# Optimization experiments

Measured on AMD Instinct MI355X. Metric: run time of the kernel, lower is better.

Reference implementation:

```python
import jax, jax.numpy as jnp
import numpy as np

N_NODES = 50000
N_EDGES = 800000
NUM_GRAPHS = 250
NODES_PER_GRAPH = 200  # max_len for to_dense_batch
IN_DIM = 128
H1 = 128
H2 = 128
LSTM_H = 128
OUT_DIM = 2
NEG_SLOPE = 0.2  # PyG GATConv default leaky relu slope


def setup_inputs() -> dict:
    key = jax.random.key(0)
    ks = jax.random.split(key, 16)
    x = jax.random.normal(ks[0], (N_NODES, IN_DIM), dtype=jnp.float32)
    edge_index = jax.random.randint(ks[1], (2, N_EDGES), 0, N_NODES, dtype=jnp.int32)
    batch = (jnp.arange(N_NODES, dtype=jnp.int32) // NODES_PER_GRAPH)
    g = lambda k, shp, fan: jax.random.normal(k, shp, dtype=jnp.float32) / np.sqrt(fan)
    return {
        "x": x,
        "edge_index": edge_index,
        "batch": batch,
        "W_gat": g(ks[2], (IN_DIM, H1), IN_DIM),
        "a_src": g(ks[3], (H1,), H1),
        "a_dst": g(ks[4], (H1,), H1),
        "b_gat": jnp.zeros((H1,), jnp.float32),
        "W_gcn": g(ks[5], (H1, H2), H1),
        "b_gcn": jnp.zeros((H2,), jnp.float32),
        "W_ih": g(ks[6], (4 * LSTM_H, H2), H2),
        "W_hh": g(ks[7], (4 * LSTM_H, LSTM_H), LSTM_H),
        "b_ih": jnp.zeros((4 * LSTM_H,), jnp.float32),
        "b_hh": jnp.zeros((4 * LSTM_H,), jnp.float32),
        "W_fc": g(ks[8], (LSTM_H, OUT_DIM), LSTM_H),
        "b_fc": jnp.zeros((OUT_DIM,), jnp.float32),
    }


def _add_self_loops(edge_index, n):
    loop = jnp.arange(n, dtype=edge_index.dtype)
    src = jnp.concatenate([edge_index[0], loop])
    dst = jnp.concatenate([edge_index[1], loop])
    return src, dst


def _gat_conv(x, edge_index, W, a_src, a_dst, b):
    n = x.shape[0]
    h = x @ W                                  # [N, H1]
    src, dst = _add_self_loops(edge_index, n)
    alpha_s = h @ a_src                        # [N]
    alpha_d = h @ a_dst
    e = alpha_s[src] + alpha_d[dst]            # [E+N]
    e = jnp.where(e > 0, e, NEG_SLOPE * e)     # leaky relu
    # softmax over edges sharing the same destination node
    m = jax.ops.segment_max(e, dst, num_segments=n)
    ex = jnp.exp(e - m[dst])
    denom = jax.ops.segment_sum(ex, dst, num_segments=n)
    alpha = ex / denom[dst]
    out = jax.ops.segment_sum(h[src] * alpha[:, None], dst, num_segments=n)
    return out + b


def _gcn_conv(x, edge_index, W, b):
    n = x.shape[0]
    h = x @ W                                  # [N, H2]
    src, dst = _add_self_loops(edge_index, n)
    deg = jax.ops.segment_sum(jnp.ones_like(dst, dtype=h.dtype), dst, num_segments=n)
    dinv = jax.lax.rsqrt(jnp.maximum(deg, 1.0))
    coef = dinv[src] * dinv[dst]               # symmetric normalization
    out = jax.ops.segment_sum(h[src] * coef[:, None], dst, num_segments=n)
    return out + b


def _to_dense_batch(x, batch, num_graphs, max_len):
    n = x.shape[0]
    ones = jnp.ones((n,), jnp.int32)
    counts = jax.ops.segment_sum(ones, batch, num_segments=num_graphs)
    starts = jnp.cumsum(counts) - counts
    pos = jnp.arange(n, dtype=jnp.int32) - starts[batch]
    padded = jnp.zeros((num_graphs, max_len, x.shape[1]), x.dtype)
    padded = padded.at[batch, pos].set(x)
    return padded, counts


def _lstm_last_hidden(padded, lengths, W_ih, W_hh, b_ih, b_hh):
    B, T, D = padded.shape
    H = W_hh.shape[1]
    xs = jnp.swapaxes(padded, 0, 1)            # [T, B, D]

    def step(carry, x_t):
        h, c = carry
        gates = x_t @ W_ih.T + b_ih + h @ W_hh.T + b_hh
        i, f, g, o = jnp.split(gates, 4, axis=-1)
        c = jax.nn.sigmoid(f) * c + jax.nn.sigmoid(i) * jnp.tanh(g)
        h = jax.nn.sigmoid(o) * jnp.tanh(c)
        return (h, c), h

    init = (jnp.zeros((B, H), padded.dtype), jnp.zeros((B, H), padded.dtype))
    _, hs = jax.lax.scan(step, init, xs)       # hs: [T, B, H]
    # packed-sequence semantics: hidden state at each graph's last valid step
    return hs[lengths - 1, jnp.arange(B)]


def reference(x, edge_index, batch, W_gat, a_src, a_dst, b_gat, W_gcn, b_gcn,
              W_ih, W_hh, b_ih, b_hh, W_fc, b_fc):
    h = jax.nn.relu(_gat_conv(x, edge_index, W_gat, a_src, a_dst, b_gat))
    h = jax.nn.relu(_gcn_conv(h, edge_index, W_gcn, b_gcn))
    padded, lengths = _to_dense_batch(h, batch, NUM_GRAPHS, NODES_PER_GRAPH)
    g_rep = _lstm_last_hidden(padded, lengths, W_ih, W_hh, b_ih, b_hh)
    return g_rep @ W_fc + b_fc
```

## Files before the change

kernel.cpp:

```cpp
#include <hip/hip_runtime.h>
#include <cstddef>

#define NN 50000
#define NE 800000
#define NG 250
#define TT 200
#define DD 128
#define GH 512
#define NEG_SLOPE 0.2f
#define NCHUNK 4
#define CLEN 50
#define CAP 128
#define PSTRIDE 136

typedef __attribute__((ext_vector_type(8))) short bf16x8;
typedef __attribute__((ext_vector_type(4))) float f32x4;

static __device__ __forceinline__ float fsig(float x) { return 1.0f / (1.0f + __expf(-x)); }
static __device__ __forceinline__ float ftanh(float x) {
    float e = __expf(2.0f * x);
    return 1.0f - 2.0f / (e + 1.0f);
}
static __device__ __forceinline__ unsigned short f2bf(float f) {
    unsigned int u = __float_as_uint(f);
    return (unsigned short)((u + 0x7fffu + ((u >> 16) & 1u)) >> 16);
}
static __device__ __forceinline__ float bf2f(unsigned short b) {
    return __uint_as_float(((unsigned int)b) << 16);
}

static __device__ __forceinline__ void gll16(const float* src, float* ldsdst) {
    __builtin_amdgcn_global_load_lds(
        (const __attribute__((address_space(1))) void*)src,
        (__attribute__((address_space(3))) void*)ldsdst, 16, 0, 0);
}

__global__ void k_init(int* cnt, int* gstart, int n, int ng1) {
    int i = blockIdx.x * 256 + threadIdx.x;
    if (i < n) cnt[i] = 1;
    if (i < ng1) gstart[i] = n;
}

__global__ void k_transpose2(const float* __restrict__ inA, float* __restrict__ outA,
                             const float* __restrict__ inB, float* __restrict__ outB) {
    int b = blockIdx.x, k = threadIdx.x;
    if (b < DD) outA[b * DD + k] = inA[k * DD + b];
    else { int n = b - DD; outB[n * DD + k] = inB[k * DD + n]; }
}

__global__ __launch_bounds__(256) void k_gemm(
    const float* __restrict__ A, const float* __restrict__ B, float* __restrict__ C,
    int M, int N, int t0, int clen, int rowsPerGraph,
    const float* __restrict__ bias1, const float* __restrict__ bias2,
    unsigned short* __restrict__ Cbf,
    float* __restrict__ as_out, float* __restrict__ ad_out,
    const float* __restrict__ a_src, const float* __restrict__ a_dst)
{
    __shared__ float4 As[2][1024];
    __shared__ float4 Bs[2][1024];
    const int tid = threadIdx.x;
    const int wv = tid >> 6;
    const int m0 = blockIdx.x * 128, n0 = blockIdx.y * 128;
    const int tr = tid >> 4, tc = tid & 15;

    float acc[8][8];
    #pragma unroll
    for (int i = 0; i < 8; ++i)
        #pragma unroll
        for (int j = 0; j < 8; ++j) acc[i][j] = 0.f;

    auto stageA = [&](int buf, int k0) {
        #pragma unroll
        for (int it = 0; it < 4; ++it) {
            int f4 = it * 256 + tid;
            int r = f4 >> 3;
            int c4s = (f4 & 7) ^ (r & 7);
            int gr = m0 + r;
            float* dst = (float*)&As[buf][it * 256 + wv * 64];
            if (gr < M) {
                int flat = (gr / clen) * rowsPerGraph + t0 + (gr % clen);
                gll16(A + (size_t)flat * DD + k0 + c4s * 4, dst);
            }
        }
    };
    auto stageB = [&](int buf, int k0) {
        #pragma unroll
        for (int it = 0; it < 4; ++it) {
            int f4 = it * 256 + tid;
            int r = f4 >> 3;
            int c4s = (f4 & 7) ^ (r & 7);
            int gn = n0 + r;
            float* dst = (float*)&Bs[buf][it * 256 + wv * 64];
            if (gn < N) gll16(B + (size_t)gn * DD + k0 + c4s * 4, dst);
        }
    };

    stageA(0, 0); stageB(0, 0);
    __syncthreads();
    int buf = 0;
    const int axor = tr & 7;
    const int bxor = tc & 7;
    for (int ks = 0; ks < 4; ++ks) {
        if (ks < 3) { stageA(buf ^ 1, (ks + 1) * 32); stageB(buf ^ 1, (ks + 1) * 32); }
        const float4* Af = &As[buf][0];
        const float4* Bf = &Bs[buf][0];
        #pragma unroll 1
        for (int k4 = 0; k4 < 8; ++k4) {
            float4 a[8], b[8];
            #pragma unroll
            for (int i = 0; i < 8; ++i) a[i] = Af[(tr + i * 16) * 8 + (k4 ^ axor)];
            #pragma unroll
            for (int j = 0; j < 8; ++j) b[j] = Bf[(tc + j * 16) * 8 + (k4 ^ bxor)];
            #pragma unroll
            for (int i = 0; i < 8; ++i)
                #pragma unroll
                for (int j = 0; j < 8; ++j)
                    acc[i][j] += a[i].x * b[j].x + a[i].y * b[j].y + a[i].z * b[j].z + a[i].w * b[j].w;
        }
        __syncthreads();
        buf ^= 1;
    }

    if (as_out) {
        float asv[8], adv[8];
        #pragma unroll
        for (int j = 0; j < 8; ++j) { asv[j] = a_src[tc + 16 * j]; adv[j] = a_dst[tc + 16 * j]; }
        #pragma unroll
        for (int i = 0; i < 8; ++i) {
            float s = 0.f, d = 0.f;
            #pragma unroll
            for (int j = 0; j < 8; ++j) { s += acc[i][j] * asv[j]; d += acc[i][j] * adv[j]; }
            #pragma unroll
            for (int off = 1; off < 16; off <<= 1) { s += __shfl_xor(s, off); d += __shfl_xor(d, off); }
            int gr = m0 + tr + i * 16;
            if (tc == 0 && gr < M) { as_out[gr] = s; ad_out[gr] = d; }
        }
    }

    #pragma unroll
    for (int i = 0; i < 8; ++i) {
        int gr = m0 + tr + i * 16;
        if (gr >= M) continue;
        #pragma unroll
        for (int j = 0; j < 8; ++j) {
            int gn = n0 + tc + j * 16;
            if (gn >= N) continue;
            float v = acc[i][j];
            if (bias1) v += bias1[gn];
            if (bias2) v += bias2[gn];
            if (Cbf) Cbf[(size_t)gr * N + gn] = f2bf(v);
            else     C[(size_t)gr * N + gn] = v;
        }
    }
}

__global__ __launch_bounds__(256) void k_gemm_mx(
    const float* __restrict__ A, const float* __restrict__ Bw, float* __restrict__ C,
    int M, int N, const float* __restrict__ bias1, const float* __restrict__ bias2)
{
    __shared__ float4 As[4096];
    const int tid = threadIdx.x;
    const int wv = tid >> 6;
    const int l = tid & 63;
    const int m0 = blockIdx.x * 128, n0 = blockIdx.y * 128;
    const int wr = (wv >> 1) * 64, wc = (wv & 1) * 64;
    const int lr = l & 15, kg = l >> 4;

    #pragma unroll
    for (int it = 0; it < 16; ++it) {
        int f4 = it * 256 + tid;
        int r = f4 >> 5, c4 = f4 & 31;
        int c4s = c4 ^ (r & 7);
        int gr = m0 + r;
        float* dst = (float*)&As[it * 256 + wv * 64];
        if (gr < M) gll16(A + (size_t)gr * DD + c4s * 4, dst);
    }

    bf16x8 bh[4][4];
    #pragma unroll
    for (int ct = 0; ct < 4; ++ct) {
        const float* brow = Bw + (size_t)(n0 + wc + ct * 16 + lr) * DD;
        #pragma unroll
        for (int ks = 0; ks < 4; ++ks) {
            float4 f0 = *(const float4*)(brow + ks * 32 + kg * 8);
            float4 f1 = *(const float4*)(brow + ks * 32 + kg * 8 + 4);
            float ff[8] = {f0.x, f0.y, f0.z, f0.w, f1.x, f1.y, f1.z, f1.w};
            #pragma unroll
            for (int j = 0; j < 8; ++j) bh[ct][ks][j] = (short)f2bf(ff[j]);
        }
    }
    __syncthreads();

    f32x4 acc[4][4];
    #pragma unroll
    for (int rt = 0; rt < 4; ++rt)
        #pragma unroll
        for (int ct = 0; ct < 4; ++ct) acc[rt][ct] = (f32x4){0.f, 0.f, 0.f, 0.f};

    #pragma unroll 1
    for (int ks = 0; ks < 4; ++ks) {
        bf16x8 ahi[4], alo[4];
        #pragma unroll
        for (int rt = 0; rt < 4; ++rt) {
            int row = wr + rt * 16 + lr;
            int qb = ks * 8 + kg * 2;
            float4 f0 = As[row * 32 + (qb ^ (row & 7))];
            float4 f1 = As[row * 32 + ((qb + 1) ^ (row & 7))];
            float ff[8] = {f0.x, f0.y, f0.z, f0.w, f1.x, f1.y, f1.z, f1.w};
            #pragma unroll
            for (int j = 0; j < 8; ++j) {
                unsigned short hi = f2bf(ff[j]);
                ahi[rt][j] = (short)hi;
                alo[rt][j] = (short)f2bf(ff[j] - bf2f(hi));
            }
        }
        #pragma unroll
        for (int rt = 0; rt < 4; ++rt)
            #pragma unroll
            for (int ct = 0; ct < 4; ++ct) {
                acc[rt][ct] = __builtin_amdgcn_mfma_f32_16x16x32_bf16(ahi[rt], bh[ct][ks], acc[rt][ct], 0, 0, 0);
                acc[rt][ct] = __builtin_amdgcn_mfma_f32_16x16x32_bf16(alo[rt], bh[ct][ks], acc[rt][ct], 0, 0, 0);
            }
    }

    #pragma unroll
    for (int ct = 0; ct < 4; ++ct) {
        const float* brow = Bw + (size_t)(n0 + wc + ct * 16 + lr) * DD;
        #pragma unroll
        for (int ks = 0; ks < 4; ++ks) {
            float4 f0 = *(const float4*)(brow + ks * 32 + kg * 8);
            float4 f1 = *(const float4*)(brow + ks * 32 + kg * 8 + 4);
            float ff[8] = {f0.x, f0.y, f0.z, f0.w, f1.x, f1.y, f1.z, f1.w};
            #pragma unroll
            for (int j = 0; j < 8; ++j)
                bh[ct][ks][j] = (short)f2bf(ff[j] - bf2f(f2bf(ff[j])));
        }
    }

    #pragma unroll 1
    for (int ks = 0; ks < 4; ++ks) {
        bf16x8 ahi[4];
        #pragma unroll
        for (int rt = 0; rt < 4; ++rt) {
            int row = wr + rt * 16 + lr;
            int qb = ks * 8 + kg * 2;
            float4 f0 = As[row * 32 + (qb ^ (row & 7))];
            float4 f1 = As[row * 32 + ((qb + 1) ^ (row & 7))];
            float ff[8] = {f0.x, f0.y, f0.z, f0.w, f1.x, f1.y, f1.z, f1.w};
            #pragma unroll
            for (int j = 0; j < 8; ++j) ahi[rt][j] = (short)f2bf(ff[j]);
        }
        #pragma unroll
        for (int rt = 0; rt < 4; ++rt)
            #pragma unroll
            for (int ct = 0; ct < 4; ++ct)
                acc[rt][ct] = __builtin_amdgcn_mfma_f32_16x16x32_bf16(ahi[rt], bh[ct][ks], acc[rt][ct], 0, 0, 0);
    }

    #pragma unroll
    for (int ct = 0; ct < 4; ++ct) {
        int col = n0 + wc + ct * 16 + lr;
        float bsum = bias1[col] + bias2[col];
        #pragma unroll
        for (int rt = 0; rt < 4; ++rt) {
            #pragma unroll
            for (int r = 0; r < 4; ++r) {
                int row = m0 + wr + rt * 16 + kg * 4 + r;
                if (row < M) C[(size_t)row * N + col] = acc[rt][ct][r] + bsum;
            }
        }
    }
}

__global__ void k_hist(const int* __restrict__ ei, int* cnt, int E) {
    int e = blockIdx.x * 256 + threadIdx.x;
    if (e < E) atomicAdd(&cnt[ei[E + e]], 1);
}

__global__ __launch_bounds__(256) void k_scan1(const int* __restrict__ cnt, int* __restrict__ fill,
                                               int* __restrict__ bsum, int n) {
    __shared__ int wsum[4];
    int tid = threadIdx.x, lane = tid & 63, wv = tid >> 6;
    int i = blockIdx.x * 256 + tid;
    int v = (i < n) ? cnt[i] : 0;
    int sc = v;
    #pragma unroll
    for (int off = 1; off < 64; off <<= 1) {
        int t = __shfl_up(sc, off);
        if (lane >= off) sc += t;
    }
    if (lane == 63) wsum[wv] = sc;
    __syncthreads();
    int base = 0;
    if (wv > 0) base += wsum[0];
    if (wv > 1) base += wsum[1];
    if (wv > 2) base += wsum[2];
    if (i < n) fill[i] = base + sc - v;
    if (tid == 255) bsum[blockIdx.x] = base + sc;
}
__global__ __launch_bounds__(256) void k_scan2(int* __restrict__ bsum, int nb) {
    __shared__ int wsum[4];
    int tid = threadIdx.x, lane = tid & 63, wv = tid >> 6;
    int v = (tid < nb) ? bsum[tid] : 0;
    int sc = v;
    #pragma unroll
    for (int off = 1; off < 64; off <<= 1) {
        int t = __shfl_up(sc, off);
        if (lane >= off) sc += t;
    }
    if (lane == 63) wsum[wv] = sc;
    __syncthreads();
    int base = 0;
    if (wv > 0) base += wsum[0];
    if (wv > 1) base += wsum[1];
    if (wv > 2) base += wsum[2];
    if (tid < nb) bsum[tid] = base + sc - v;
}
__global__ void k_scan3(const int* __restrict__ bsum, const int* __restrict__ cnt,
                        int* __restrict__ rp, int* __restrict__ fill,
                        float* __restrict__ dinv, const int* __restrict__ batch,
                        int* __restrict__ gstart, int n) {
    int i = blockIdx.x * 256 + threadIdx.x;
    if (i >= n) return;
    int v = fill[i] + bsum[blockIdx.x];
    rp[i] = v;
    fill[i] = v;
    if (i == n - 1) rp[n] = v + cnt[i];
    dinv[i] = rsqrtf(fmaxf((float)cnt[i], 1.0f));
    int b = batch[i];
    if (i == 0 || batch[i - 1] != b) gstart[b] = i;
}

__global__ void k_fill(const int* __restrict__ ei, int* fill, int* esrc, int E, int N) {
    int i = blockIdx.x * 256 + threadIdx.x;
    if (i < E) {
        int s = ei[i], d = ei[E + i];
        int slot = atomicAdd(&fill[d], 1);
        esrc[slot] = s;
    } else if (i < E + N) {
        int v = i - E;
        int slot = atomicAdd(&fill[v], 1);
        esrc[slot] = v;
    }
}

__global__ __launch_bounds__(256) void k_gat(
    const unsigned int* __restrict__ h1b,
    const float* __restrict__ as, const float* __restrict__ ad_,
    const int* __restrict__ rp, const int* __restrict__ esrc,
    const float* __restrict__ bias, float* __restrict__ out, int n)
{
    __shared__ float2 ws_sh[4][CAP];
    int wv = threadIdx.x >> 6;
    int node = blockIdx.x * 4 + wv;
    int lane = threadIdx.x & 63;
    if (node >= n) return;
    int r0 = rp[node], r1 = rp[node + 1];
    int deg = r1 - r0;
    float adv = ad_[node];

    float sum = 0.f;
    for (int base = 0; base < deg; base += 64) {
        int idx = base + lane;
        float ex = 0.f;
        if (idx < deg) {
            int s = esrc[r0 + idx];
            float e = as[s] + adv;
            e = e > 0.f ? e : NEG_SLOPE * e;
            ex = __expf(e);
            if (idx < CAP) ws_sh[wv][idx] = make_float2(ex, __int_as_float(s));
        }
        sum += ex;
    }
    #pragma unroll
    for (int off = 1; off < 64; off <<= 1) sum += __shfl_xor(sum, off);
    float inv = 1.0f / sum;

    int nser = deg < CAP ? deg : CAP;
    int npad = (nser + 7) & ~7;
    for (int p = nser + lane; p < npad; p += 64)
        ws_sh[wv][p] = make_float2(0.f, __int_as_float(0));

    float ax = 0.f, ay = 0.f;
    float wa[8]; unsigned int va[8];
    #pragma unroll
    for (int u = 0; u < 8; ++u) {
        float2 t = ws_sh[wv][u];
        wa[u] = t.x; va[u] = h1b[(size_t)__float_as_int(t.y) * 64 + lane];
    }
    #pragma unroll 1
    for (int idx = 8; idx < npad; idx += 8) {
        float wb[8]; unsigned int vb[8];
        #pragma unroll
        for (int u = 0; u < 8; ++u) {
            float2 t = ws_sh[wv][idx + u];
            wb[u] = t.x; vb[u] = h1b[(size_t)__float_as_int(t.y) * 64 + lane];
        }
        #pragma unroll
        for (int u = 0; u < 8; ++u) {
            ax += wa[u] * __uint_as_float(va[u] << 16);
            ay += wa[u] * __uint_as_float(va[u] & 0xffff0000u);
        }
        #pragma unroll
        for (int u = 0; u < 8; ++u) { wa[u] = wb[u]; va[u] = vb[u]; }
    }
    #pragma unroll
    for (int u = 0; u < 8; ++u) {
        ax += wa[u] * __uint_as_float(va[u] << 16);
        ay += wa[u] * __uint_as_float(va[u] & 0xffff0000u);
    }

    for (int j = r0 + CAP; j < r1; ++j) {
        int s = esrc[j];
        float e = as[s] + adv;
        e = e > 0.f ? e : NEG_SLOPE * e;
        float w = __expf(e);
        unsigned int v = h1b[(size_t)s * 64 + lane];
        ax += w * __uint_as_float(v << 16);
        ay += w * __uint_as_float(v & 0xffff0000u);
    }
    float2 bv = *(const float2*)(bias + 2 * lane);
    float2 o;
    o.x = fmaxf(ax * inv + bv.x, 0.f);
    o.y = fmaxf(ay * inv + bv.y, 0.f);
    *(float2*)(out + (size_t)node * DD + 2 * lane) = o;
}

__global__ __launch_bounds__(256) void k_gcn(
    const unsigned int* __restrict__ h2b, const float* __restrict__ dinv,
    const int* __restrict__ rp, const int* __restrict__ esrc,
    const float* __restrict__ bias, const int* __restrict__ batch,
    const int* __restrict__ gstart, float* __restrict__ padded, int n)
{
    __shared__ float2 cs_sh[4][CAP];
    int wv = threadIdx.x >> 6;
    int node = blockIdx.x * 4 + wv;
    int lane = threadIdx.x & 63;
    if (node >= n) return;
    int r0 = rp[node], r1 = rp[node + 1];
    int deg = r1 - r0;
    float dn = dinv[node];

    for (int base = 0; base < deg; base += 64) {
        int idx = base + lane;
        if (idx < deg && idx < CAP) {
            int s = esrc[r0 + idx];
            cs_sh[wv][idx] = make_float2(dinv[s], __int_as_float(s));
        }
    }
    int nser = deg < CAP ? deg : CAP;
    int npad = (nser + 7) & ~7;
    for (int p = nser + lane; p < npad; p += 64)
        cs_sh[wv][p] = make_float2(0.f, __int_as_float(0));
    __syncthreads();

    float ax = 0.f, ay = 0.f;
    float wa[8]; unsigned int va[8];
    #pragma unroll
    for (int u = 0; u < 8; ++u) {
        float2 t = cs_sh[wv][u];
        wa[u] = t.x; va[u] = h2b[(size_t)__float_as_int(t.y) * 64 + lane];
    }
    #pragma unroll 1
    for (int idx = 8; idx < npad; idx += 8) {
        float wb[8]; unsigned int vb[8];
        #pragma unroll
        for (int u = 0; u < 8; ++u) {
            float2 t = cs_sh[wv][idx + u];
            wb[u] = t.x; vb[u] = h2b[(size_t)__float_as_int(t.y) * 64 + lane];
        }
        #pragma unroll
        for (int u = 0; u < 8; ++u) {
            ax += wa[u] * __uint_as_float(va[u] << 16);
            ay += wa[u] * __uint_as_float(va[u] & 0xffff0000u);
        }
        #pragma unroll
        for (int u = 0; u < 8; ++u) { wa[u] = wb[u]; va[u] = vb[u]; }
    }
    #pragma unroll
    for (int u = 0; u < 8; ++u) {
        ax += wa[u] * __uint_as_float(va[u] << 16);
        ay += wa[u] * __uint_as_float(va[u] & 0xffff0000u);
    }

    for (int j = r0 + CAP; j < r1; ++j) {
        int s = esrc[j];
        float c = dinv[s];
        unsigned int v = h2b[(size_t)s * 64 + lane];
        ax += c * __uint_as_float(v << 16);
        ay += c * __uint_as_float(v & 0xffff0000u);
    }
    int g = batch[node];
    if (g < 0 || g >= NG) return;
    int p = node - gstart[g];
    if (p < 0 || p >= TT) return;
    float2 bv = *(const float2*)(bias + 2 * lane);
    float2 o;
    o.x = fmaxf(ax * dn + bv.x, 0.f);
    o.y = fmaxf(ay * dn + bv.y, 0.f);
    *(float2*)(padded + ((size_t)g * TT + p) * DD + 2 * lane) = o;
}

__global__ __launch_bounds__(512) void k_lstm(
    const float* __restrict__ xw, const float* __restrict__ Whh,
    const int* __restrict__ gstart,
    float* __restrict__ hstate, float* __restrict__ cstate,
    float* __restrict__ grep, int t0, int clen)
{
    int g = blockIdx.x, tid = threadIdx.x;
    __shared__ __align__(16) float h_sh[DD];
    __shared__ __align__(16) float part[4][4 * PSTRIDE];

    const int seg = tid >> 7;
    const int gq  = tid & 127;
    const int qt  = gq >> 5;
    const int ub  = (gq & 31) * 4;
    const int u   = tid >> 2;
    const int q   = tid & 3;
    const int lane = tid & 63;
    const int qbase = lane & ~3;

    float4 w[4][8];
    #pragma unroll
    for (int g4 = 0; g4 < 4; ++g4)
        #pragma unroll
        for (int i = 0; i < 8; ++i)
            w[g4][i] = *(const float4*)(Whh + (size_t)(4 * gq + g4) * DD + seg * 32 + i * 4);

    float creg = 0.f, hn = 0.f;
    if (t0 == 0) {
        if (tid < DD) h_sh[tid] = 0.f;
    } else {
        creg = cstate[g * DD + u];
        hn = hstate[g * DD + u];
        if (q == 0) h_sh[u] = hn;
    }
    int take = gstart[g + 1] - gstart[g] - 1;
    if (take < 0) take = 0;
    if (take > TT - 1) take = TT - 1;
    __syncthreads();

    const float* xb = xw + (size_t)g * clen * GH + q * DD + u;
    float xv = xb[0];

    for (int t = t0; t < t0 + clen; ++t) {
        int rel = t - t0;
        float xvn = 0.f;
        if (rel + 1 < clen) xvn = xb[(size_t)(rel + 1) * GH];

        float4 hseg[8];
        #pragma unroll
        for (int i = 0; i < 8; ++i) hseg[i] = *(const float4*)(h_sh + seg * 32 + i * 4);
        float p0 = 0.f, p1 = 0.f, p2 = 0.f, p3 = 0.f;
        #pragma unroll
        for (int i = 0; i < 8; ++i) {
            float4 h4 = hseg[i];
            p0 += h4.x * w[0][i].x + h4.y * w[0][i].y + h4.z * w[0][i].z + h4.w * w[0][i].w;
            p1 += h4.x * w[1][i].x + h4.y * w[1][i].y + h4.z * w[1][i].z + h4.w * w[1][i].w;
            p2 += h4.x * w[2][i].x + h4.y * w[2][i].y + h4.z * w[2][i].z + h4.w * w[2][i].w;
            p3 += h4.x * w[3][i].x + h4.y * w[3][i].y + h4.z * w[3][i].z + h4.w * w[3][i].w;
        }
        *(float4*)(&part[seg][qt * PSTRIDE + ub]) = make_float4(p0, p1, p2, p3);
        __syncthreads();

        int pidx = q * PSTRIDE + u;
        float G = xv + part[0][pidx] + part[1][pidx] + part[2][pidx] + part[3][pidx];
        float a = (q == 2) ? 2.f : -1.f;
        float e = __expf(a * G);
        float act = (q == 2) ? (1.f - 2.f / (e + 1.f)) : (1.f / (1.f + e));
        float ai = __shfl(act, qbase + 0);
        float af = __shfl(act, qbase + 1);
        float ag = __shfl(act, qbase + 2);
        float ao = __shfl(act, qbase + 3);
        creg = af * creg + ai * ag;
        hn = ao * ftanh(creg);
        if (q == 0) {
            h_sh[u] = hn;
            if (t == take) grep[g * DD + u] = hn;
        }
        xv = xvn;
        __syncthreads();
    }
    if (q == 0) { hstate[g * DD + u] = hn; cstate[g * DD + u] = creg; }
}

__global__ void k_fc(const float* __restrict__ grep, const float* __restrict__ Wfc,
                     const float* __restrict__ bfc, float* __restrict__ out, int G) {
    int i = blockIdx.x * 256 + threadIdx.x;
    if (i >= G * 2) return;
    int g = i >> 1, o = i & 1;
    float acc = bfc[o];
    for (int d = 0; d < DD; ++d) acc += grep[g * DD + d] * Wfc[d * 2 + o];
    out[i] = acc;
}

extern "C" void kernel_launch(void* const* d_in, const int* in_sizes, int n_in,
                              void* d_out, int out_size, void* d_ws, size_t ws_size,
                              hipStream_t stream) {
    const float* x     = (const float*)d_in[0];
    const int*   ei    = (const int*)d_in[1];
    const int*   batch = (const int*)d_in[2];
    const float* Wgat  = (const float*)d_in[3];
    const float* a_src = (const float*)d_in[4];
    const float* a_dst = (const float*)d_in[5];
    const float* b_gat = (const float*)d_in[6];
    const float* Wgcn  = (const float*)d_in[7];
    const float* b_gcn = (const float*)d_in[8];
    const float* Wih   = (const float*)d_in[9];
    const float* Whh   = (const float*)d_in[10];
    const float* b_ih  = (const float*)d_in[11];
    const float* b_hh  = (const float*)d_in[12];
    const float* Wfc   = (const float*)d_in[13];
    const float* b_fc  = (const float*)d_in[14];
    float* out = (float*)d_out;

    float* ws = (float*)d_ws;
    const size_t F = (size_t)NN * DD;
    unsigned short* h1b = (unsigned short*)ws;
    unsigned short* h2b = (unsigned short*)ws;
    float* xwChunk = ws;
    float* gato   = ws + F;
    float* padded = ws + F;
    size_t off = 2 * F;
    float* alpha_s = ws + off; off += 50048;
    float* alpha_d = ws + off; off += 50048;
    float* dinv    = ws + off; off += 50048;
    int*   cnt     = (int*)(ws + off); off += 50048;
    int*   rp      = (int*)(ws + off); off += 50056;
    int*   fill    = (int*)(ws + off); off += 50048;
    int*   esrc    = (int*)(ws + off); off += 850048;
    int*   bsum    = (int*)(ws + off); off += 256;
    int*   gstart  = (int*)(ws + off); off += 256;
    float* grep    = ws + off; off += 32000;
    float* hstate  = ws + off; off += 32000;
    float* cstate  = ws + off; off += 32000;
    float* WgatT   = ws + off; off += 16384;
    float* WgcnT   = ws + off; off += 16384;
    const size_t xwBigFloats = (size_t)NG * TT * GH;
    float* xwBig = ws + off;
    const bool big = ws_size >= (off + xwBigFloats) * sizeof(float);

    k_transpose2<<<256, 128, 0, stream>>>(Wgat, WgatT, Wgcn, WgcnT);

    k_gemm<<<dim3(391, 1), 256, 0, stream>>>(x, WgatT, nullptr, NN, DD, 0, TT, TT,
                                             nullptr, nullptr, h1b,
                                             alpha_s, alpha_d, a_src, a_dst);

    k_init<<<196, 256, 0, stream>>>(cnt, gstart, NN, NG + 1);
    k_hist<<<3125, 256, 0, stream>>>(ei, cnt, NE);
    k_scan1<<<196, 256, 0, stream>>>(cnt, fill, bsum, NN);
    k_scan2<<<1, 256, 0, stream>>>(bsum, 196);
    k_scan3<<<196, 256, 0, stream>>>(bsum, cnt, rp, fill, dinv, batch, gstart, NN);
    k_fill<<<3321, 256, 0, stream>>>(ei, fill, esrc, NE, NN);

    k_gat<<<12500, 256, 0, stream>>>((const unsigned int*)h1b, alpha_s, alpha_d,
                                     rp, esrc, b_gat, gato, NN);

    k_gemm<<<dim3(391, 1), 256, 0, stream>>>(gato, WgcnT, nullptr, NN, DD, 0, TT, TT,
                                             nullptr, nullptr, h2b,
                                             nullptr, nullptr, nullptr, nullptr);

    k_gcn<<<12500, 256, 0, stream>>>((const unsigned int*)h2b, dinv, rp, esrc,
                                     b_gcn, batch, gstart, padded, NN);

    if (big) {
        k_gemm_mx<<<dim3(391, 4), 256, 0, stream>>>(padded, Wih, xwBig, NG * TT, GH,
                                                    b_ih, b_hh);
        k_lstm<<<NG, 512, 0, stream>>>(xwBig, Whh, gstart, hstate, cstate, grep, 0, TT);
    } else {
        for (int c = 0; c < NCHUNK; ++c) {
            int t0 = c * CLEN;
            k_gemm<<<dim3(98, 4), 256, 0, stream>>>(padded, Wih, xwChunk, NG * CLEN, GH,
                                                    t0, CLEN, TT, b_ih, b_hh,
                                                    nullptr, nullptr, nullptr, nullptr, nullptr);
            k_lstm<<<NG, 512, 0, stream>>>(xwChunk, Whh, gstart, hstate, cstate, grep, t0, CLEN);
        }
    }

    k_fc<<<2, 256, 0, stream>>>(grep, Wfc, b_fc, out, NG);
}
```

Baseline: 550.7 us.

## Use 1024-thread LSTM recurrence and dedicated 128-wide split-bf16 node GEMM

```diff
diff --git a/kernel.cpp b/kernel.cpp
--- a/kernel.cpp
+++ b/kernel.cpp
@@ -272,6 +272,136 @@
     }
 }
 
+__global__ __launch_bounds__(256) void k_gemm_mx128(
+    const float* __restrict__ A, const float* __restrict__ Bw,
+    unsigned short* __restrict__ Cbf, int M,
+    float* __restrict__ as_out, float* __restrict__ ad_out,
+    const float* __restrict__ a_src, const float* __restrict__ a_dst)
+{
+    __shared__ float4 As[4096];
+    const int tid = threadIdx.x;
+    const int wv = tid >> 6;
+    const int l = tid & 63;
+    const int lr = l & 15, kg = l >> 4;
+    const int m0 = blockIdx.x * 128;
+    const int rowbase = wv * 32;
+
+    #pragma unroll
+    for (int it = 0; it < 16; ++it) {
+        int f4 = it * 256 + tid;
+        int r = f4 >> 5, c4 = f4 & 31;
+        int c4s = c4 ^ (r & 7);
+        int gr = m0 + r;
+        float* dst = (float*)&As[it * 256 + wv * 64];
+        if (gr < M) gll16(A + (size_t)gr * DD + c4s * 4, dst);
+    }
+    __syncthreads();
+
+    f32x4 acc[2][8];
+    #pragma unroll
+    for (int rt = 0; rt < 2; ++rt)
+        #pragma unroll
+        for (int ct = 0; ct < 8; ++ct) acc[rt][ct] = (f32x4){0.f, 0.f, 0.f, 0.f};
+
+    #pragma unroll 1
+    for (int ks = 0; ks < 4; ++ks) {
+        bf16x8 bh[8];
+        #pragma unroll
+        for (int ct = 0; ct < 8; ++ct) {
+            const float* brow = Bw + (size_t)(ct * 16 + lr) * DD + ks * 32 + kg * 8;
+            float4 f0 = *(const float4*)brow;
+            float4 f1 = *(const float4*)(brow + 4);
+            float ff[8] = {f0.x, f0.y, f0.z, f0.w, f1.x, f1.y, f1.z, f1.w};
+            #pragma unroll
+            for (int j = 0; j < 8; ++j) bh[ct][j] = (short)f2bf(ff[j]);
+        }
+        bf16x8 ahi[2], alo[2];
+        #pragma unroll
+        for (int rt = 0; rt < 2; ++rt) {
+            int row = rowbase + rt * 16 + lr;
+            int qb = ks * 8 + kg * 2;
+            float4 f0 = As[row * 32 + (qb ^ (row & 7))];
+            float4 f1 = As[row * 32 + ((qb + 1) ^ (row & 7))];
+            float ff[8] = {f0.x, f0.y, f0.z, f0.w, f1.x, f1.y, f1.z, f1.w};
+            #pragma unroll
+            for (int j = 0; j < 8; ++j) {
+                unsigned short hi = f2bf(ff[j]);
+                ahi[rt][j] = (short)hi;
+                alo[rt][j] = (short)f2bf(ff[j] - bf2f(hi));
+            }
+        }
+        #pragma unroll
+        for (int rt = 0; rt < 2; ++rt)
+            #pragma unroll
+            for (int ct = 0; ct < 8; ++ct) {
+                acc[rt][ct] = __builtin_amdgcn_mfma_f32_16x16x32_bf16(ahi[rt], bh[ct], acc[rt][ct], 0, 0, 0);
+                acc[rt][ct] = __builtin_amdgcn_mfma_f32_16x16x32_bf16(alo[rt], bh[ct], acc[rt][ct], 0, 0, 0);
+            }
+    }
+    #pragma unroll 1
+    for (int ks = 0; ks < 4; ++ks) {
+        bf16x8 bl[8];
+        #pragma unroll
+        for (int ct = 0; ct < 8; ++ct) {
+            const float* brow = Bw + (size_t)(ct * 16 + lr) * DD + ks * 32 + kg * 8;
+            float4 f0 = *(const float4*)brow;
+            float4 f1 = *(const float4*)(brow + 4);
+            float ff[8] = {f0.x, f0.y, f0.z, f0.w, f1.x, f1.y, f1.z, f1.w};
+            #pragma unroll
+            for (int j = 0; j < 8; ++j)
+                bl[ct][j] = (short)f2bf(ff[j] - bf2f(f2bf(ff[j])));
+        }
+        bf16x8 ahi[2];
+        #pragma unroll
+        for (int rt = 0; rt < 2; ++rt) {
+            int row = rowbase + rt * 16 + lr;
+            int qb = ks * 8 + kg * 2;
+            float4 f0 = As[row * 32 + (qb ^ (row & 7))];
+            float4 f1 = As[row * 32 + ((qb + 1) ^ (row & 7))];
+            float ff[8] = {f0.x, f0.y, f0.z, f0.w, f1.x, f1.y, f1.z, f1.w};
+            #pragma unroll
+            for (int j = 0; j < 8; ++j) ahi[rt][j] = (short)f2bf(ff[j]);
+        }
+        #pragma unroll
+        for (int rt = 0; rt < 2; ++rt)
+            #pragma unroll
+            for (int ct = 0; ct < 8; ++ct)
+                acc[rt][ct] = __builtin_amdgcn_mfma_f32_16x16x32_bf16(ahi[rt], bl[ct], acc[rt][ct], 0, 0, 0);
+    }
+
+    #pragma unroll
+    for (int rt = 0; rt < 2; ++rt)
+        #pragma unroll
+        for (int ct = 0; ct < 8; ++ct) {
+            int row = m0 + rowbase + rt * 16 + kg * 4;
+            int col = ct * 16 + lr;
+            #pragma unroll
+            for (int r = 0; r < 4; ++r)
+                if (row + r < M) Cbf[(size_t)(row + r) * DD + col] = f2bf(acc[rt][ct][r]);
+        }
+    if (as_out) {
+        #pragma unroll
+        for (int rt = 0; rt < 2; ++rt)
+            #pragma unroll
+            for (int r = 0; r < 4; ++r) {
+                float s = 0.f, d = 0.f;
+                #pragma unroll
+                for (int ct = 0; ct < 8; ++ct) {
+                    int col = ct * 16 + lr;
+                    s += acc[rt][ct][r] * a_src[col];
+                    d += acc[rt][ct][r] * a_dst[col];
+                }
+                #pragma unroll
+                for (int off = 1; off < 16; off <<= 1) {
+                    s += __shfl_xor(s, off);
+                    d += __shfl_xor(d, off);
+                }
+                int row = m0 + rowbase + rt * 16 + kg * 4 + r;
+                if (lr == 0 && row < M) { as_out[row] = s; ad_out[row] = d; }
+            }
+    }
+}
+
 __global__ void k_hist(const int* __restrict__ ei, int* cnt, int E) {
     int e = blockIdx.x * 256 + threadIdx.x;
     if (e < E) atomicAdd(&cnt[ei[E + e]], 1);
@@ -499,6 +629,84 @@
     o.x = fmaxf(ax * dn + bv.x, 0.f);
     o.y = fmaxf(ay * dn + bv.y, 0.f);
     *(float2*)(padded + ((size_t)g * TT + p) * DD + 2 * lane) = o;
+}
+
+__global__ __launch_bounds__(1024) void k_lstm8(
+    const float* __restrict__ xw,
+    const float* __restrict__ Whh,
+    const int* __restrict__ gstart,
+    float* __restrict__ grep)
+{
+    int g = blockIdx.x, tid = threadIdx.x;
+    __shared__ __align__(16) float h_sh[DD];
+    __shared__ __align__(16) float part[8][4 * PSTRIDE];
+
+    const int seg = tid >> 7;
+    const int gq  = tid & 127;
+    const int qt  = gq >> 5;
+    const int ub  = (gq & 31) * 4;
+    const int u   = tid >> 2;
+    const int q   = tid & 3;
+    const int lane = tid & 63;
+    const int qbase = lane & ~3;
+
+    float4 w[4][4];
+    #pragma unroll
+    for (int g4 = 0; g4 < 4; ++g4)
+        #pragma unroll
+        for (int i = 0; i < 4; ++i)
+            w[g4][i] = *(const float4*)(Whh + (size_t)(4 * gq + g4) * DD + seg * 16 + i * 4);
+
+    float creg = 0.f, hn = 0.f;
+    if (tid < DD) h_sh[tid] = 0.f;
+    int take = gstart[g + 1] - gstart[g] - 1;
+    if (take < 0) take = 0;
+    if (take > TT - 1) take = TT - 1;
+    __syncthreads();
+
+    const float* xb = xw + (size_t)g * TT * GH + q * DD + (u & 127);
+    float xv = (tid < 512) ? xb[0] : 0.f;
+
+    for (int t = 0; t < TT; ++t) {
+        float xvn = 0.f;
+        if (tid < 512 && t + 1 < TT) xvn = xb[(size_t)(t + 1) * GH];
+
+        float4 hseg[4];
+        #pragma unroll
+        for (int i = 0; i < 4; ++i) hseg[i] = *(const float4*)(h_sh + seg * 16 + i * 4);
+        float p0 = 0.f, p1 = 0.f, p2 = 0.f, p3 = 0.f;
+        #pragma unroll
+        for (int i = 0; i < 4; ++i) {
+            float4 h4 = hseg[i];
+            p0 += h4.x * w[0][i].x + h4.y * w[0][i].y + h4.z * w[0][i].z + h4.w * w[0][i].w;
+            p1 += h4.x * w[1][i].x + h4.y * w[1][i].y + h4.z * w[1][i].z + h4.w * w[1][i].w;
+            p2 += h4.x * w[2][i].x + h4.y * w[2][i].y + h4.z * w[2][i].z + h4.w * w[2][i].w;
+            p3 += h4.x * w[3][i].x + h4.y * w[3][i].y + h4.z * w[3][i].z + h4.w * w[3][i].w;
+        }
+        *(float4*)(&part[seg][qt * PSTRIDE + ub]) = make_float4(p0, p1, p2, p3);
+        __syncthreads();
+
+        if (tid < 512) {
+            int pidx = q * PSTRIDE + u;
+            float G = xv + ((part[0][pidx] + part[1][pidx]) + (part[2][pidx] + part[3][pidx]))
+                         + ((part[4][pidx] + part[5][pidx]) + (part[6][pidx] + part[7][pidx]));
+            float a = (q == 2) ? 2.f : -1.f;
+            float e = __expf(a * G);
+            float act = (q == 2) ? (1.f - 2.f / (e + 1.f)) : (1.f / (1.f + e));
+            float ai = __shfl(act, qbase + 0);
+            float af = __shfl(act, qbase + 1);
+            float ag = __shfl(act, qbase + 2);
+            float ao = __shfl(act, qbase + 3);
+            creg = af * creg + ai * ag;
+            hn = ao * ftanh(creg);
+            if (q == 0) {
+                h_sh[u] = hn;
+                if (t == take) grep[g * DD + u] = hn;
+            }
+        }
+        xv = xvn;
+        __syncthreads();
+    }
 }
 
 __global__ __launch_bounds__(512) void k_lstm(
@@ -642,9 +850,14 @@
 
     k_transpose2<<<256, 128, 0, stream>>>(Wgat, WgatT, Wgcn, WgcnT);
 
-    k_gemm<<<dim3(391, 1), 256, 0, stream>>>(x, WgatT, nullptr, NN, DD, 0, TT, TT,
-                                             nullptr, nullptr, h1b,
-                                             alpha_s, alpha_d, a_src, a_dst);
+    if (big) {
+        k_gemm_mx128<<<391, 256, 0, stream>>>(x, WgatT, h1b, NN,
+                                              alpha_s, alpha_d, a_src, a_dst);
+    } else {
+        k_gemm<<<dim3(391, 1), 256, 0, stream>>>(x, WgatT, nullptr, NN, DD, 0, TT, TT,
+                                                 nullptr, nullptr, h1b,
+                                                 alpha_s, alpha_d, a_src, a_dst);
+    }
 
     k_init<<<196, 256, 0, stream>>>(cnt, gstart, NN, NG + 1);
     k_hist<<<3125, 256, 0, stream>>>(ei, cnt, NE);
@@ -656,9 +869,14 @@
     k_gat<<<12500, 256, 0, stream>>>((const unsigned int*)h1b, alpha_s, alpha_d,
                                      rp, esrc, b_gat, gato, NN);
 
-    k_gemm<<<dim3(391, 1), 256, 0, stream>>>(gato, WgcnT, nullptr, NN, DD, 0, TT, TT,
-                                             nullptr, nullptr, h2b,
-                                             nullptr, nullptr, nullptr, nullptr);
+    if (big) {
+        k_gemm_mx128<<<391, 256, 0, stream>>>(gato, WgcnT, h2b, NN,
+                                              nullptr, nullptr, nullptr, nullptr);
+    } else {
+        k_gemm<<<dim3(391, 1), 256, 0, stream>>>(gato, WgcnT, nullptr, NN, DD, 0, TT, TT,
+                                                 nullptr, nullptr, h2b,
+                                                 nullptr, nullptr, nullptr, nullptr);
+    }
 
     k_gcn<<<12500, 256, 0, stream>>>((const unsigned int*)h2b, dinv, rp, esrc,
                                      b_gcn, batch, gstart, padded, NN);
@@ -666,7 +884,7 @@
     if (big) {
         k_gemm_mx<<<dim3(391, 4), 256, 0, stream>>>(padded, Wih, xwBig, NG * TT, GH,
                                                     b_ih, b_hh);
-        k_lstm<<<NG, 512, 0, stream>>>(xwBig, Whh, gstart, hstate, cstate, grep, 0, TT);
+        k_lstm8<<<NG, 1024, 0, stream>>>(xwBig, Whh, gstart, grep);
     } else {
         for (int c = 0; c < NCHUNK; ++c) {
             int t0 = c * CLEN;
```

New measurement: 559.6 us. About the same (+1.6%).
